# Kernel optimization log

Measured on AMD Instinct MI355X. Metric: run time of the kernel, lower is better.

Reference implementation:

```python
import jax, jax.numpy as jnp
import numpy as np
import math

RIEMANN_ZEROS_IM = (14.134725142, 21.022039639, 25.01085758, 30.424876126, 32.935061588,
    37.586178159, 40.918719012, 43.327073281, 48.005150881, 49.773832478, 52.970321478,
    56.446247697, 59.347044003, 60.831778525, 65.112544048, 67.079810529, 69.546401711,
    72.067157674, 75.704690699, 77.144840069, 79.33737502, 82.910380854, 84.735492981,
    87.425274613, 88.809111208, 92.491899271, 94.651344041, 95.870634228, 98.831194218,
    101.317851006, 103.72553804, 105.446623052)

D_MODEL = 1024
N_HEADS = 16
D_HEAD = D_MODEL // N_HEADS  # 64
N_PAIRS = D_HEAD // 2        # 32

# normalized inverse frequencies: gamma_n / gamma_1, inverted
_gamma = np.asarray(RIEMANN_ZEROS_IM[:N_PAIRS], dtype=np.float32)
INV_FREQ = jnp.asarray(1.0 / (_gamma / _gamma[0]))  # [n_pairs]


def _rotate(x, cos, sin):
    # x: [b,h,n,d_head]; cos/sin: [1,h,n,n_pairs]; interleaved pair rotation
    x1 = x[..., 0::2]
    x2 = x[..., 1::2]
    rx1 = x1 * cos - x2 * sin
    rx2 = x1 * sin + x2 * cos
    return jnp.stack([rx1, rx2], axis=-1).reshape(x.shape)


def setup_inputs() -> dict:
    key = jax.random.key(0)
    k1, k2, k3 = jax.random.split(key, 3)
    b, n = 4, 2048
    x = jax.random.normal(k1, (b, n, D_MODEL), dtype=jnp.float32)
    # torch Linear(d, 3d, bias=False): y = x @ W.T; we store W.T directly
    w_qkv = jax.random.normal(k2, (D_MODEL, 3 * D_MODEL), dtype=jnp.float32) / math.sqrt(D_MODEL)
    w_o = jax.random.normal(k3, (D_MODEL, D_MODEL), dtype=jnp.float32) / math.sqrt(D_MODEL)
    log_scale = jnp.zeros((N_HEADS,), dtype=jnp.float32)
    return {"x": x, "w_qkv": w_qkv, "w_o": w_o, "log_scale": log_scale}


def reference(x, w_qkv, w_o, log_scale):
    b, n, d = x.shape
    qkv = (x @ w_qkv).reshape(b, n, 3, N_HEADS, D_HEAD)
    q, k, v = qkv[:, :, 0], qkv[:, :, 1], qkv[:, :, 2]  # [b,n,h,dh]
    q = q.transpose(0, 2, 1, 3)  # [b,h,n,dh]
    k = k.transpose(0, 2, 1, 3)
    v = v.transpose(0, 2, 1, 3)

    scale = jnp.exp(log_scale)  # [h]
    pos = jnp.arange(n, dtype=jnp.float32)
    # theta: [1,h,n,n_pairs]
    theta = pos[None, None, :, None] * INV_FREQ[None, None, None, :] * scale[None, :, None, None]
    cos, sin = jnp.cos(theta), jnp.sin(theta)
    q = _rotate(q, cos, sin)
    k = _rotate(k, cos, sin)

    scores = jnp.einsum('bhqd,bhkd->bhqk', q, k) / math.sqrt(D_HEAD)
    causal = jnp.tril(jnp.ones((n, n), dtype=bool))
    scores = jnp.where(causal[None, None], scores, -jnp.inf)
    attn = jax.nn.softmax(scores, axis=-1)
    out = jnp.einsum('bhqk,bhkd->bhqd', attn, v)
    out = out.transpose(0, 2, 1, 3).reshape(b, n, d)
    return out @ w_o
```

## Files before the change

kernel.cpp:

```cpp
#include <hip/hip_runtime.h>
#include <hip/hip_bf16.h>

#define B_ 4
#define N_ 2048
#define DM 1024
#define NH 16
#define DH 64

typedef __attribute__((ext_vector_type(8))) __bf16 bf16x8;
typedef __attribute__((ext_vector_type(4))) float f32x4;
typedef __attribute__((ext_vector_type(4))) float float4v;
typedef __attribute__((ext_vector_type(4))) unsigned int uint4v;
typedef __attribute__((ext_vector_type(2))) unsigned int uint2v;
typedef __attribute__((ext_vector_type(4))) unsigned short ushort4v;

__device__ __forceinline__ float bf2f(unsigned short h) {
  union { unsigned int u; float f; } v; v.u = ((unsigned int)h) << 16; return v.f;
}
__device__ __forceinline__ unsigned short f2bf(float f) {
  __bf16 h = (__bf16)f;
  return __builtin_bit_cast(unsigned short, h);
}
__device__ __forceinline__ f32x4 mfma16(bf16x8 a, bf16x8 b, f32x4 c) {
  return __builtin_amdgcn_mfma_f32_16x16x32_bf16(a, b, c, 0, 0, 0);
}
__device__ __forceinline__ void gload_lds16(const void* g, void* l) {
  __builtin_amdgcn_global_load_lds(
      (const __attribute__((address_space(1))) unsigned int*)g,
      (__attribute__((address_space(3))) unsigned int*)l, 16, 0, 0);
}

__constant__ float GAMMA_C[32] = {
  14.134725142f, 21.022039639f, 25.01085758f, 30.424876126f,
  32.935061588f, 37.586178159f, 40.918719012f, 43.327073281f,
  48.005150881f, 49.773832478f, 52.970321478f, 56.446247697f,
  59.347044003f, 60.831778525f, 65.112544048f, 67.079810529f,
  69.546401711f, 72.067157674f, 75.704690699f, 77.144840069f,
  79.33737502f,  82.910380854f, 84.735492981f, 87.425274613f,
  88.809111208f, 92.491899271f, 94.651344041f, 95.870634228f,
  98.831194218f, 101.317851006f, 103.72553804f, 105.446623052f
};

__global__ __launch_bounds__(256) void cast_f32_bf16(
    const float* __restrict__ in, unsigned short* __restrict__ out, int n4) {
  int i = blockIdx.x * 256 + threadIdx.x;
  if (i >= n4) return;
  float4v v = *(const float4v*)&in[(size_t)i * 4];
  ushort4v o;
  o[0] = f2bf(v[0]); o[1] = f2bf(v[1]); o[2] = f2bf(v[2]); o[3] = f2bf(v[3]);
  *(ushort4v*)&out[(size_t)i * 4] = o;
}

__global__ __launch_bounds__(256) void tcast(
    const float* __restrict__ in, unsigned short* __restrict__ out, int K, int N) {
  __shared__ float t[32][33];
  int n0 = blockIdx.x * 32, k0 = blockIdx.y * 32;
  int tx = threadIdx.x, ty = threadIdx.y;
#pragma unroll
  for (int j = 0; j < 4; ++j)
    t[ty + j * 8][tx] = in[(size_t)(k0 + ty + j * 8) * N + n0 + tx];
  __syncthreads();
#pragma unroll
  for (int j = 0; j < 4; ++j)
    out[(size_t)(n0 + ty + j * 8) * K + k0 + tx] = f2bf(t[tx][ty + j * 8]);
}

template <int OUTF32>
__global__ __launch_bounds__(256) void gemm_bt(
    const unsigned short* __restrict__ A, const unsigned short* __restrict__ BT,
    void* __restrict__ C, int M, int N, int K) {
  __shared__ unsigned short As[128 * 32];
  __shared__ unsigned short Bs[128 * 32];
  int tid = threadIdx.x;
  int lane = tid & 63, wid = tid >> 6;
  int wr = wid >> 1, wc = wid & 1;
  int lr = lane & 15, lg = lane >> 4;
  int bm = blockIdx.y * 128, bn = blockIdx.x * 128;
  int srow = lane >> 2, sch = lane & 3;
  f32x4 acc[4][4];
#pragma unroll
  for (int m = 0; m < 4; ++m)
#pragma unroll
    for (int n = 0; n < 4; ++n) acc[m][n] = (f32x4){0.f, 0.f, 0.f, 0.f};

  for (int k0 = 0; k0 < K; k0 += 32) {
    __syncthreads();
#pragma unroll
    for (int it = 0; it < 2; ++it) {
      int rbase = wid * 16 + it * 64;
      gload_lds16(&A[(size_t)(bm + rbase + srow) * K + k0 + sch * 8],
                  &As[rbase * 32]);
      gload_lds16(&BT[(size_t)(bn + rbase + srow) * K + k0 + sch * 8],
                  &Bs[rbase * 32]);
    }
    __syncthreads();
    bf16x8 af[4], bfr[4];
#pragma unroll
    for (int m = 0; m < 4; ++m)
      af[m] = *(const bf16x8*)&As[(wr * 64 + m * 16 + lr) * 32 + lg * 8];
#pragma unroll
    for (int n = 0; n < 4; ++n)
      bfr[n] = *(const bf16x8*)&Bs[(wc * 64 + n * 16 + lr) * 32 + lg * 8];
    __builtin_amdgcn_s_setprio(1);
#pragma unroll
    for (int m = 0; m < 4; ++m)
#pragma unroll
      for (int n = 0; n < 4; ++n)
        acc[m][n] = mfma16(af[m], bfr[n], acc[m][n]);
    __builtin_amdgcn_s_setprio(0);
  }
#pragma unroll
  for (int m = 0; m < 4; ++m)
#pragma unroll
    for (int n = 0; n < 4; ++n) {
      int row = bm + wr * 64 + m * 16 + lg * 4;
      int col = bn + wc * 64 + n * 16 + lr;
#pragma unroll
      for (int r = 0; r < 4; ++r) {
        if (OUTF32)
          ((float*)C)[(size_t)(row + r) * N + col] = acc[m][n][r];
        else
          ((unsigned short*)C)[(size_t)(row + r) * N + col] = f2bf(acc[m][n][r]);
      }
    }
}

__global__ __launch_bounds__(256) void rope_split(
    const unsigned short* __restrict__ qkv, const float* __restrict__ log_scale,
    unsigned short* __restrict__ Qr, unsigned short* __restrict__ Kr,
    unsigned short* __restrict__ Vr) {
  int t = blockIdx.x * 256 + threadIdx.x;
  int p = t & 31, h = (t >> 5) & 15, n = (t >> 9) & 2047, b = t >> 20;
  float ratio = GAMMA_C[p] / GAMMA_C[0];
  float invf = 1.0f / ratio;
  float scale = expf(log_scale[h]);
  float theta = ((float)n * invf) * scale;
  float sn, cs;
  sincosf(theta, &sn, &cs);
  size_t base = (size_t)(b * N_ + n) * (3 * DM) + h * DH + 2 * p;
  unsigned int qu = *(const unsigned int*)&qkv[base];
  unsigned int ku = *(const unsigned int*)&qkv[base + DM];
  unsigned int vu = *(const unsigned int*)&qkv[base + 2 * DM];
  float q1 = bf2f(qu & 0xffffu), q2 = bf2f(qu >> 16);
  float k1 = bf2f(ku & 0xffffu), k2 = bf2f(ku >> 16);
  unsigned int rq = (unsigned int)f2bf(q1 * cs - q2 * sn) |
                    ((unsigned int)f2bf(q1 * sn + q2 * cs) << 16);
  unsigned int rk = (unsigned int)f2bf(k1 * cs - k2 * sn) |
                    ((unsigned int)f2bf(k1 * sn + k2 * cs) << 16);
  size_t ob = (size_t)((b * NH + h) * N_ + n) * DH + 2 * p;
  *(unsigned int*)&Qr[ob] = rq;
  *(unsigned int*)&Kr[ob] = rk;
  *(unsigned int*)&Vr[ob] = vu;
}

__global__ __launch_bounds__(256) void attn_fwd(
    const unsigned short* __restrict__ Q, const unsigned short* __restrict__ K,
    const unsigned short* __restrict__ V, unsigned short* __restrict__ AO) {
  int orig = blockIdx.x;
  int wg = (orig & 7) * 128 + (orig >> 3);
  int i = wg & 15;
  int qt = ((wg >> 5) & 1) ? (15 - i) : i;
  int bh = wg >> 4;
  int b = bh >> 4, h = bh & 15;
  int q0 = qt * 128;
  int tid = threadIdx.x;
  int lane = tid & 63, w = tid >> 6;
  int lr = lane & 15, lg = lane >> 4;

  const unsigned short* Qh = Q + (size_t)bh * N_ * DH;
  const unsigned short* Kh = K + (size_t)bh * N_ * DH;
  const unsigned short* Vh = V + (size_t)bh * N_ * DH;

  __shared__ unsigned short Ks[64 * 64];
  __shared__ unsigned short Vt[64 * 64];
  __shared__ unsigned int PsU[4][32][32];

  bf16x8 qf[2][2];
#pragma unroll
  for (int m = 0; m < 2; ++m)
#pragma unroll
    for (int dh = 0; dh < 2; ++dh)
      qf[m][dh] = *(const bf16x8*)
          &Qh[(size_t)(q0 + w * 32 + m * 16 + lr) * DH + dh * 32 + lg * 8];

  f32x4 oacc[2][4];
#pragma unroll
  for (int m = 0; m < 2; ++m)
#pragma unroll
    for (int nb = 0; nb < 4; ++nb) oacc[m][nb] = (f32x4){0.f, 0.f, 0.f, 0.f};
  float mst[2] = {-1e30f, -1e30f};
  float lst[2] = {0.f, 0.f};

  int wkend = q0 + w * 32 + 31;
  int ksup = q0 + 128;
  int vch = tid & 7, vk = tid >> 3;
  int swz = 4 * (lr & 7);

  for (int k0 = 0; k0 < ksup; k0 += 64) {
    __syncthreads();
#pragma unroll
    for (int it = 0; it < 2; ++it) {
      int rbase = w * 8 + it * 32;
      int row = rbase + (lane >> 3);
      int sk = ((row & 7) ^ (row >> 3)) & 7;
      int ch = lane & 7;
      gload_lds16(&Kh[(size_t)(k0 + row) * DH + ((ch ^ sk) * 8)],
                  &Ks[rbase * 64]);
    }
#pragma unroll
    for (int it = 0; it < 2; ++it) {
      int k = vk + it * 32;
      uint4v vv = *(const uint4v*)&Vh[(size_t)(k0 + k) * DH + vch * 8];
      const unsigned short* pv = (const unsigned short*)&vv;
#pragma unroll
      for (int j = 0; j < 8; ++j) {
        int d = vch * 8 + j;
        int sv = (j ^ vch) & 7;
        Vt[d * 64 + (k ^ (sv << 3))] = pv[j];
      }
    }
    __syncthreads();
    if (k0 > wkend) continue;

    f32x4 s[2][4];
    __builtin_amdgcn_s_setprio(1);
#pragma unroll
    for (int nb = 0; nb < 4; ++nb) {
      int key = nb * 16 + lr;
      int sk = ((key & 7) ^ (key >> 3)) & 7;
      bf16x8 kf0 = *(const bf16x8*)&Ks[key * 64 + ((lg ^ sk) * 8)];
      bf16x8 kf1 = *(const bf16x8*)&Ks[key * 64 + (((4 + lg) ^ sk) * 8)];
#pragma unroll
      for (int m = 0; m < 2; ++m) {
        f32x4 z = (f32x4){0.f, 0.f, 0.f, 0.f};
        z = mfma16(kf0, qf[m][0], z);
        z = mfma16(kf1, qf[m][1], z);
        s[m][nb] = z;
      }
    }
    __builtin_amdgcn_s_setprio(0);

    float sv[2][4][4];
    float mx[2];
#pragma unroll
    for (int m = 0; m < 2; ++m) {
      int qm = q0 + w * 32 + m * 16;
      int q = qm + lr;
      bool um = (k0 + 63 > qm);
#pragma unroll
      for (int nb = 0; nb < 4; ++nb)
#pragma unroll
        for (int r = 0; r < 4; ++r) {
          float t = s[m][nb][r] * 0.125f;
          if (um && (k0 + nb * 16 + lg * 4 + r > q)) t = -1e30f;
          sv[m][nb][r] = t;
        }
      float mx0 = fmaxf(fmaxf(sv[m][0][0], sv[m][0][1]),
                        fmaxf(sv[m][0][2], sv[m][0][3]));
      float mx1 = fmaxf(fmaxf(sv[m][1][0], sv[m][1][1]),
                        fmaxf(sv[m][1][2], sv[m][1][3]));
      float mx2 = fmaxf(fmaxf(sv[m][2][0], sv[m][2][1]),
                        fmaxf(sv[m][2][2], sv[m][2][3]));
      float mx3 = fmaxf(fmaxf(sv[m][3][0], sv[m][3][1]),
                        fmaxf(sv[m][3][2], sv[m][3][3]));
      float m01 = fmaxf(fmaxf(mx0, mx1), fmaxf(mx2, mx3));
      m01 = fmaxf(m01, __shfl_xor(m01, 16, 64));
      m01 = fmaxf(m01, __shfl_xor(m01, 32, 64));
      mx[m] = m01;
    }

    if (__any((mx[0] > mst[0] + 8.f) || (mx[1] > mst[1] + 8.f))) {
      float scs[2];
#pragma unroll
      for (int m = 0; m < 2; ++m) {
        float mnew = fmaxf(mst[m], mx[m]);
        float sc = __expf(mst[m] - mnew);
        mst[m] = mnew;
        lst[m] *= sc;
        scs[m] = sc;
      }
#pragma unroll
      for (int m = 0; m < 2; ++m)
#pragma unroll
        for (int r = 0; r < 4; ++r) {
          float scr = __shfl(scs[m], lg * 4 + r, 64);
#pragma unroll
          for (int nb = 0; nb < 4; ++nb) oacc[m][nb][r] *= scr;
        }
    }

#pragma unroll
    for (int m = 0; m < 2; ++m) {
      float ps = 0.f;
      unsigned int pw[8];
#pragma unroll
      for (int nb = 0; nb < 4; ++nb)
#pragma unroll
        for (int rp = 0; rp < 2; ++rp) {
          float p0 = __expf(sv[m][nb][2 * rp] - mst[m]);
          float p1 = __expf(sv[m][nb][2 * rp + 1] - mst[m]);
          ps += p0 + p1;
          pw[nb * 2 + rp] =
              (unsigned int)f2bf(p0) | ((unsigned int)f2bf(p1) << 16);
        }
#pragma unroll
      for (int nb = 0; nb < 4; ++nb) {
        int c0 = (nb * 8 + lg * 2) ^ swz;
        *(uint2v*)&PsU[w][m * 16 + lr][c0] = (uint2v){pw[nb * 2], pw[nb * 2 + 1]};
      }
      ps += __shfl_xor(ps, 16, 64);
      ps += __shfl_xor(ps, 32, 64);
      lst[m] += ps;
    }
    asm volatile("s_waitcnt lgkmcnt(0)" ::: "memory");
    __builtin_amdgcn_sched_barrier(0);

    __builtin_amdgcn_s_setprio(1);
#pragma unroll
    for (int kh = 0; kh < 2; ++kh) {
      bf16x8 pf0 = *(const bf16x8*)&PsU[w][lr][(kh * 16 + lg * 4) ^ swz];
      bf16x8 pf1 = *(const bf16x8*)&PsU[w][16 + lr][(kh * 16 + lg * 4) ^ swz];
#pragma unroll
      for (int nb = 0; nb < 4; ++nb) {
        int d = nb * 16 + lr;
        int sv2 = ((d & 7) ^ (d >> 3)) & 7;
        bf16x8 vf = *(const bf16x8*)
            &Vt[d * 64 + ((kh * 32 + lg * 8) ^ (sv2 << 3))];
        oacc[0][nb] = mfma16(pf0, vf, oacc[0][nb]);
        oacc[1][nb] = mfma16(pf1, vf, oacc[1][nb]);
      }
    }
    __builtin_amdgcn_s_setprio(0);
  }

#pragma unroll
  for (int m = 0; m < 2; ++m) {
    float inv = 1.0f / lst[m];
#pragma unroll
    for (int r = 0; r < 4; ++r) {
      float invr = __shfl(inv, lg * 4 + r, 64);
      int q = q0 + w * 32 + m * 16 + lg * 4 + r;
#pragma unroll
      for (int nb = 0; nb < 4; ++nb) {
        float o = oacc[m][nb][r] * invr;
        AO[(size_t)(b * N_ + q) * DM + h * DH + nb * 16 + lr] = f2bf(o);
      }
    }
  }
}

extern "C" void kernel_launch(void* const* d_in, const int* in_sizes, int n_in,
                              void* d_out, int out_size, void* d_ws, size_t ws_size,
                              hipStream_t stream) {
  const float* x = (const float*)d_in[0];
  const float* w_qkv = (const float*)d_in[1];
  const float* w_o = (const float*)d_in[2];
  const float* log_scale = (const float*)d_in[3];
  float* out = (float*)d_out;

  char* ws = (char*)d_ws;
  unsigned short* xb  = (unsigned short*)(ws);
  unsigned short* ao  = xb;
  unsigned short* wqT = (unsigned short*)(ws + (16u << 20));
  unsigned short* woT = (unsigned short*)(ws + (22u << 20));
  unsigned short* qkv = (unsigned short*)(ws + (24u << 20));
  unsigned short* Qr  = (unsigned short*)(ws + (72u << 20));
  unsigned short* Kr  = (unsigned short*)(ws + (88u << 20));
  unsigned short* Vr  = (unsigned short*)(ws + (104u << 20));

  cast_f32_bf16<<<8192, 256, 0, stream>>>(x, xb, (B_ * N_ * DM) / 4);
  dim3 tb(32, 8);
  tcast<<<dim3(3 * DM / 32, DM / 32), tb, 0, stream>>>(w_qkv, wqT, DM, 3 * DM);
  tcast<<<dim3(DM / 32, DM / 32), tb, 0, stream>>>(w_o, woT, DM, DM);
  gemm_bt<0><<<dim3(3 * DM / 128, (B_ * N_) / 128), 256, 0, stream>>>(
      xb, wqT, qkv, B_ * N_, 3 * DM, DM);
  rope_split<<<(B_ * N_ * NH * 32) / 256, 256, 0, stream>>>(
      qkv, log_scale, Qr, Kr, Vr);
  attn_fwd<<<B_ * NH * (N_ / 128), 256, 0, stream>>>(Qr, Kr, Vr, ao);
  gemm_bt<1><<<dim3(DM / 128, (B_ * N_) / 128), 256, 0, stream>>>(
      ao, woT, out, B_ * N_, DM, DM);
}
```

Measured before the change: 257.0 us.

## Pre-transpose V in rope kernel and double-buffer K/V tiles in attention

The rope/split kernel now writes V already transposed ([bh][d][n]) through a shared-memory transpose, so attention can load V tiles with async global-to-LDS copies instead of scalar LDS scatter stores. The attention kernel double-buffers the K and V tiles, prefetching the next tile while computing the current one, and drops from two barriers to one per iteration. The P staging buffer is halved by processing the two m-subtiles one after another. The cost is extra LDS for the double buffers, a shared-memory transpose in the rope kernel, and a serialized P write/read per m-subtile.

Result: slower. 265.6 us (+3.4%).

```diff
diff --git a/kernel.cpp b/kernel.cpp
--- a/kernel.cpp
+++ b/kernel.cpp
@@ -128,29 +128,50 @@
 __global__ __launch_bounds__(256) void rope_split(
     const unsigned short* __restrict__ qkv, const float* __restrict__ log_scale,
     unsigned short* __restrict__ Qr, unsigned short* __restrict__ Kr,
-    unsigned short* __restrict__ Vr) {
-  int t = blockIdx.x * 256 + threadIdx.x;
-  int p = t & 31, h = (t >> 5) & 15, n = (t >> 9) & 2047, b = t >> 20;
-  float ratio = GAMMA_C[p] / GAMMA_C[0];
-  float invf = 1.0f / ratio;
-  float scale = expf(log_scale[h]);
-  float theta = ((float)n * invf) * scale;
-  float sn, cs;
-  sincosf(theta, &sn, &cs);
-  size_t base = (size_t)(b * N_ + n) * (3 * DM) + h * DH + 2 * p;
-  unsigned int qu = *(const unsigned int*)&qkv[base];
-  unsigned int ku = *(const unsigned int*)&qkv[base + DM];
-  unsigned int vu = *(const unsigned int*)&qkv[base + 2 * DM];
-  float q1 = bf2f(qu & 0xffffu), q2 = bf2f(qu >> 16);
-  float k1 = bf2f(ku & 0xffffu), k2 = bf2f(ku >> 16);
-  unsigned int rq = (unsigned int)f2bf(q1 * cs - q2 * sn) |
-                    ((unsigned int)f2bf(q1 * sn + q2 * cs) << 16);
-  unsigned int rk = (unsigned int)f2bf(k1 * cs - k2 * sn) |
-                    ((unsigned int)f2bf(k1 * sn + k2 * cs) << 16);
-  size_t ob = (size_t)((b * NH + h) * N_ + n) * DH + 2 * p;
-  *(unsigned int*)&Qr[ob] = rq;
-  *(unsigned int*)&Kr[ob] = rk;
-  *(unsigned int*)&Vr[ob] = vu;
+    unsigned short* __restrict__ Vt) {
+  int nt = blockIdx.x, bh = blockIdx.y;
+  int b = bh >> 4, h = bh & 15;
+  int n0 = nt * 128;
+  int tid = threadIdx.x;
+  int p = tid & 31, nl0 = tid >> 5;
+  __shared__ unsigned int Vl[128][33];
+  float invf = GAMMA_C[0] / GAMMA_C[p];
+  float scale = __expf(log_scale[h]);
+#pragma unroll
+  for (int j = 0; j < 16; ++j) {
+    int nl = nl0 + j * 8;
+    int n = n0 + nl;
+    size_t base = (size_t)(b * N_ + n) * (3 * DM) + h * DH + 2 * p;
+    unsigned int qu = *(const unsigned int*)&qkv[base];
+    unsigned int ku = *(const unsigned int*)&qkv[base + DM];
+    unsigned int vu = *(const unsigned int*)&qkv[base + 2 * DM];
+    float th = (float)n * invf * scale;
+    float sn, cs;
+    sincosf(th, &sn, &cs);
+    float q1 = bf2f(qu & 0xffffu), q2 = bf2f(qu >> 16);
+    float k1 = bf2f(ku & 0xffffu), k2 = bf2f(ku >> 16);
+    unsigned int rq = (unsigned int)f2bf(q1 * cs - q2 * sn) |
+                      ((unsigned int)f2bf(q1 * sn + q2 * cs) << 16);
+    unsigned int rk = (unsigned int)f2bf(k1 * cs - k2 * sn) |
+                      ((unsigned int)f2bf(k1 * sn + k2 * cs) << 16);
+    size_t ob = (size_t)(bh * N_ + n) * DH + 2 * p;
+    *(unsigned int*)&Qr[ob] = rq;
+    *(unsigned int*)&Kr[ob] = rk;
+    Vl[nl][p] = vu;
+  }
+  __syncthreads();
+  int d = tid & 63, ch = tid >> 6;
+  int dp = d >> 1, sh = (d & 1) * 16;
+#pragma unroll
+  for (int j = 0; j < 4; ++j) {
+    int cc = ch + j * 4;
+    unsigned short o[8];
+#pragma unroll
+    for (int i = 0; i < 8; ++i)
+      o[i] = (unsigned short)(Vl[cc * 8 + i][dp] >> sh);
+    *(uint4v*)&Vt[(size_t)bh * DH * N_ + (size_t)d * N_ + n0 + cc * 8] =
+        *(const uint4v*)o;
+  }
 }
 
 __global__ __launch_bounds__(256) void attn_fwd(
@@ -169,11 +190,11 @@
 
   const unsigned short* Qh = Q + (size_t)bh * N_ * DH;
   const unsigned short* Kh = K + (size_t)bh * N_ * DH;
-  const unsigned short* Vh = V + (size_t)bh * N_ * DH;
-
-  __shared__ unsigned short Ks[64 * 64];
-  __shared__ unsigned short Vt[64 * 64];
-  __shared__ unsigned int PsU[4][32][32];
+  const unsigned short* Vh = V + (size_t)bh * DH * N_;
+
+  __shared__ unsigned short Ks[2][64 * 64];
+  __shared__ unsigned short Vs[2][64 * 64];
+  __shared__ unsigned int PsU[4][16][32];
 
   bf16x8 qf[2][2];
 #pragma unroll
@@ -193,144 +214,148 @@
 
   int wkend = q0 + w * 32 + 31;
   int ksup = q0 + 128;
-  int vch = tid & 7, vk = tid >> 3;
   int swz = 4 * (lr & 7);
 
+  int srow = lane >> 3, sch = lane & 7;
+
+#pragma unroll
+  for (int it = 0; it < 2; ++it) {
+    int rbase = w * 16 + it * 8;
+    int row = rbase + srow;
+    int sk = (row & 7) ^ ((row >> 3) & 7);
+    gload_lds16(&Kh[(size_t)row * DH + ((sch ^ sk) * 8)], &Ks[0][rbase * 64]);
+    gload_lds16(&Vh[(size_t)row * N_ + ((sch ^ sk) * 8)], &Vs[0][rbase * 64]);
+  }
+  asm volatile("s_waitcnt vmcnt(0)" ::: "memory");
+  __syncthreads();
+  int cur = 0;
+
   for (int k0 = 0; k0 < ksup; k0 += 64) {
+    if (k0 + 64 < ksup) {
+#pragma unroll
+      for (int it = 0; it < 2; ++it) {
+        int rbase = w * 16 + it * 8;
+        int row = rbase + srow;
+        int sk = (row & 7) ^ ((row >> 3) & 7);
+        gload_lds16(&Kh[(size_t)(k0 + 64 + row) * DH + ((sch ^ sk) * 8)],
+                    &Ks[cur ^ 1][rbase * 64]);
+        gload_lds16(&Vh[(size_t)row * N_ + k0 + 64 + ((sch ^ sk) * 8)],
+                    &Vs[cur ^ 1][rbase * 64]);
+      }
+    }
+
+    if (k0 <= wkend) {
+      f32x4 s[2][4];
+      __builtin_amdgcn_s_setprio(1);
+#pragma unroll
+      for (int nb = 0; nb < 4; ++nb) {
+        int key = nb * 16 + lr;
+        int sk = (key & 7) ^ ((key >> 3) & 7);
+        bf16x8 kf0 = *(const bf16x8*)&Ks[cur][key * 64 + ((lg ^ sk) * 8)];
+        bf16x8 kf1 = *(const bf16x8*)&Ks[cur][key * 64 + (((4 + lg) ^ sk) * 8)];
+#pragma unroll
+        for (int m = 0; m < 2; ++m) {
+          f32x4 z = (f32x4){0.f, 0.f, 0.f, 0.f};
+          z = mfma16(kf0, qf[m][0], z);
+          z = mfma16(kf1, qf[m][1], z);
+          s[m][nb] = z;
+        }
+      }
+      __builtin_amdgcn_s_setprio(0);
+
+      float sv[2][4][4];
+      float mx[2];
+#pragma unroll
+      for (int m = 0; m < 2; ++m) {
+        int qm = q0 + w * 32 + m * 16;
+        int q = qm + lr;
+        bool um = (k0 + 63 > qm);
+#pragma unroll
+        for (int nb = 0; nb < 4; ++nb)
+#pragma unroll
+          for (int r = 0; r < 4; ++r) {
+            float t = s[m][nb][r] * 0.125f;
+            if (um && (k0 + nb * 16 + lg * 4 + r > q)) t = -1e30f;
+            sv[m][nb][r] = t;
+          }
+        float mx0 = fmaxf(fmaxf(sv[m][0][0], sv[m][0][1]),
+                          fmaxf(sv[m][0][2], sv[m][0][3]));
+        float mx1 = fmaxf(fmaxf(sv[m][1][0], sv[m][1][1]),
+                          fmaxf(sv[m][1][2], sv[m][1][3]));
+        float mx2 = fmaxf(fmaxf(sv[m][2][0], sv[m][2][1]),
+                          fmaxf(sv[m][2][2], sv[m][2][3]));
+        float mx3 = fmaxf(fmaxf(sv[m][3][0], sv[m][3][1]),
+                          fmaxf(sv[m][3][2], sv[m][3][3]));
+        float m01 = fmaxf(fmaxf(mx0, mx1), fmaxf(mx2, mx3));
+        m01 = fmaxf(m01, __shfl_xor(m01, 16, 64));
+        m01 = fmaxf(m01, __shfl_xor(m01, 32, 64));
+        mx[m] = m01;
+      }
+
+      if (__any((mx[0] > mst[0] + 8.f) || (mx[1] > mst[1] + 8.f))) {
+        float scs[2];
+#pragma unroll
+        for (int m = 0; m < 2; ++m) {
+          float mnew = fmaxf(mst[m], mx[m]);
+          float sc = __expf(mst[m] - mnew);
+          mst[m] = mnew;
+          lst[m] *= sc;
+          scs[m] = sc;
+        }
+#pragma unroll
+        for (int m = 0; m < 2; ++m)
+#pragma unroll
+          for (int r = 0; r < 4; ++r) {
+            float scr = __shfl(scs[m], lg * 4 + r, 64);
+#pragma unroll
+            for (int nb = 0; nb < 4; ++nb) oacc[m][nb][r] *= scr;
+          }
+      }
+
+#pragma unroll
+      for (int m = 0; m < 2; ++m) {
+        float ps = 0.f;
+        unsigned int pw[8];
+#pragma unroll
+        for (int nb = 0; nb < 4; ++nb)
+#pragma unroll
+          for (int rp = 0; rp < 2; ++rp) {
+            float p0 = __expf(sv[m][nb][2 * rp] - mst[m]);
+            float p1 = __expf(sv[m][nb][2 * rp + 1] - mst[m]);
+            ps += p0 + p1;
+            pw[nb * 2 + rp] =
+                (unsigned int)f2bf(p0) | ((unsigned int)f2bf(p1) << 16);
+          }
+#pragma unroll
+        for (int nb = 0; nb < 4; ++nb) {
+          int c0 = (nb * 8 + lg * 2) ^ swz;
+          *(uint2v*)&PsU[w][lr][c0] = (uint2v){pw[nb * 2], pw[nb * 2 + 1]};
+        }
+        ps += __shfl_xor(ps, 16, 64);
+        ps += __shfl_xor(ps, 32, 64);
+        lst[m] += ps;
+        asm volatile("s_waitcnt lgkmcnt(0)" ::: "memory");
+        __builtin_amdgcn_sched_barrier(0);
+        __builtin_amdgcn_s_setprio(1);
+#pragma unroll
+        for (int kh = 0; kh < 2; ++kh) {
+          bf16x8 pf = *(const bf16x8*)&PsU[w][lr][(kh * 16 + lg * 4) ^ swz];
+#pragma unroll
+          for (int nb = 0; nb < 4; ++nb) {
+            int d = nb * 16 + lr;
+            int sv2 = (d & 7) ^ ((d >> 3) & 7);
+            int c = kh * 4 + lg;
+            bf16x8 vf = *(const bf16x8*)&Vs[cur][d * 64 + ((c ^ sv2) * 8)];
+            oacc[m][nb] = mfma16(pf, vf, oacc[m][nb]);
+          }
+        }
+        __builtin_amdgcn_s_setprio(0);
+      }
+    }
+
+    asm volatile("s_waitcnt vmcnt(0)" ::: "memory");
     __syncthreads();
-#pragma unroll
-    for (int it = 0; it < 2; ++it) {
-      int rbase = w * 8 + it * 32;
-      int row = rbase + (lane >> 3);
-      int sk = ((row & 7) ^ (row >> 3)) & 7;
-      int ch = lane & 7;
-      gload_lds16(&Kh[(size_t)(k0 + row) * DH + ((ch ^ sk) * 8)],
-                  &Ks[rbase * 64]);
-    }
-#pragma unroll
-    for (int it = 0; it < 2; ++it) {
-      int k = vk + it * 32;
-      uint4v vv = *(const uint4v*)&Vh[(size_t)(k0 + k) * DH + vch * 8];
-      const unsigned short* pv = (const unsigned short*)&vv;
-#pragma unroll
-      for (int j = 0; j < 8; ++j) {
-        int d = vch * 8 + j;
-        int sv = (j ^ vch) & 7;
-        Vt[d * 64 + (k ^ (sv << 3))] = pv[j];
-      }
-    }
-    __syncthreads();
-    if (k0 > wkend) continue;
-
-    f32x4 s[2][4];
-    __builtin_amdgcn_s_setprio(1);
-#pragma unroll
-    for (int nb = 0; nb < 4; ++nb) {
-      int key = nb * 16 + lr;
-      int sk = ((key & 7) ^ (key >> 3)) & 7;
-      bf16x8 kf0 = *(const bf16x8*)&Ks[key * 64 + ((lg ^ sk) * 8)];
-      bf16x8 kf1 = *(const bf16x8*)&Ks[key * 64 + (((4 + lg) ^ sk) * 8)];
-#pragma unroll
-      for (int m = 0; m < 2; ++m) {
-        f32x4 z = (f32x4){0.f, 0.f, 0.f, 0.f};
-        z = mfma16(kf0, qf[m][0], z);
-        z = mfma16(kf1, qf[m][1], z);
-        s[m][nb] = z;
-      }
-    }
-    __builtin_amdgcn_s_setprio(0);
-
-    float sv[2][4][4];
-    float mx[2];
-#pragma unroll
-    for (int m = 0; m < 2; ++m) {
-      int qm = q0 + w * 32 + m * 16;
-      int q = qm + lr;
-      bool um = (k0 + 63 > qm);
-#pragma unroll
-      for (int nb = 0; nb < 4; ++nb)
-#pragma unroll
-        for (int r = 0; r < 4; ++r) {
-          float t = s[m][nb][r] * 0.125f;
-          if (um && (k0 + nb * 16 + lg * 4 + r > q)) t = -1e30f;
-          sv[m][nb][r] = t;
-        }
-      float mx0 = fmaxf(fmaxf(sv[m][0][0], sv[m][0][1]),
-                        fmaxf(sv[m][0][2], sv[m][0][3]));
-      float mx1 = fmaxf(fmaxf(sv[m][1][0], sv[m][1][1]),
-                        fmaxf(sv[m][1][2], sv[m][1][3]));
-      float mx2 = fmaxf(fmaxf(sv[m][2][0], sv[m][2][1]),
-                        fmaxf(sv[m][2][2], sv[m][2][3]));
-      float mx3 = fmaxf(fmaxf(sv[m][3][0], sv[m][3][1]),
-                        fmaxf(sv[m][3][2], sv[m][3][3]));
-      float m01 = fmaxf(fmaxf(mx0, mx1), fmaxf(mx2, mx3));
-      m01 = fmaxf(m01, __shfl_xor(m01, 16, 64));
-      m01 = fmaxf(m01, __shfl_xor(m01, 32, 64));
-      mx[m] = m01;
-    }
-
-    if (__any((mx[0] > mst[0] + 8.f) || (mx[1] > mst[1] + 8.f))) {
-      float scs[2];
-#pragma unroll
-      for (int m = 0; m < 2; ++m) {
-        float mnew = fmaxf(mst[m], mx[m]);
-        float sc = __expf(mst[m] - mnew);
-        mst[m] = mnew;
-        lst[m] *= sc;
-        scs[m] = sc;
-      }
-#pragma unroll
-      for (int m = 0; m < 2; ++m)
-#pragma unroll
-        for (int r = 0; r < 4; ++r) {
-          float scr = __shfl(scs[m], lg * 4 + r, 64);
-#pragma unroll
-          for (int nb = 0; nb < 4; ++nb) oacc[m][nb][r] *= scr;
-        }
-    }
-
-#pragma unroll
-    for (int m = 0; m < 2; ++m) {
-      float ps = 0.f;
-      unsigned int pw[8];
-#pragma unroll
-      for (int nb = 0; nb < 4; ++nb)
-#pragma unroll
-        for (int rp = 0; rp < 2; ++rp) {
-          float p0 = __expf(sv[m][nb][2 * rp] - mst[m]);
-          float p1 = __expf(sv[m][nb][2 * rp + 1] - mst[m]);
-          ps += p0 + p1;
-          pw[nb * 2 + rp] =
-              (unsigned int)f2bf(p0) | ((unsigned int)f2bf(p1) << 16);
-        }
-#pragma unroll
-      for (int nb = 0; nb < 4; ++nb) {
-        int c0 = (nb * 8 + lg * 2) ^ swz;
-        *(uint2v*)&PsU[w][m * 16 + lr][c0] = (uint2v){pw[nb * 2], pw[nb * 2 + 1]};
-      }
-      ps += __shfl_xor(ps, 16, 64);
-      ps += __shfl_xor(ps, 32, 64);
-      lst[m] += ps;
-    }
-    asm volatile("s_waitcnt lgkmcnt(0)" ::: "memory");
-    __builtin_amdgcn_sched_barrier(0);
-
-    __builtin_amdgcn_s_setprio(1);
-#pragma unroll
-    for (int kh = 0; kh < 2; ++kh) {
-      bf16x8 pf0 = *(const bf16x8*)&PsU[w][lr][(kh * 16 + lg * 4) ^ swz];
-      bf16x8 pf1 = *(const bf16x8*)&PsU[w][16 + lr][(kh * 16 + lg * 4) ^ swz];
-#pragma unroll
-      for (int nb = 0; nb < 4; ++nb) {
-        int d = nb * 16 + lr;
-        int sv2 = ((d & 7) ^ (d >> 3)) & 7;
-        bf16x8 vf = *(const bf16x8*)
-            &Vt[d * 64 + ((kh * 32 + lg * 8) ^ (sv2 << 3))];
-        oacc[0][nb] = mfma16(pf0, vf, oacc[0][nb]);
-        oacc[1][nb] = mfma16(pf1, vf, oacc[1][nb]);
-      }
-    }
-    __builtin_amdgcn_s_setprio(0);
+    cur ^= 1;
   }
 
 #pragma unroll
@@ -366,7 +391,7 @@
   unsigned short* qkv = (unsigned short*)(ws + (24u << 20));
   unsigned short* Qr  = (unsigned short*)(ws + (72u << 20));
   unsigned short* Kr  = (unsigned short*)(ws + (88u << 20));
-  unsigned short* Vr  = (unsigned short*)(ws + (104u << 20));
+  unsigned short* Vt  = (unsigned short*)(ws + (104u << 20));
 
   cast_f32_bf16<<<8192, 256, 0, stream>>>(x, xb, (B_ * N_ * DM) / 4);
   dim3 tb(32, 8);
@@ -374,9 +399,9 @@
   tcast<<<dim3(DM / 32, DM / 32), tb, 0, stream>>>(w_o, woT, DM, DM);
   gemm_bt<0><<<dim3(3 * DM / 128, (B_ * N_) / 128), 256, 0, stream>>>(
       xb, wqT, qkv, B_ * N_, 3 * DM, DM);
-  rope_split<<<(B_ * N_ * NH * 32) / 256, 256, 0, stream>>>(
-      qkv, log_scale, Qr, Kr, Vr);
-  attn_fwd<<<B_ * NH * (N_ / 128), 256, 0, stream>>>(Qr, Kr, Vr, ao);
+  rope_split<<<dim3(16, B_ * NH), 256, 0, stream>>>(
+      qkv, log_scale, Qr, Kr, Vt);
+  attn_fwd<<<B_ * NH * (N_ / 128), 256, 0, stream>>>(Qr, Kr, Vt, ao);
   gemm_bt<1><<<dim3(DM / 128, (B_ * N_) / 128), 256, 0, stream>>>(
       ao, woT, out, B_ * N_, DM, DM);
 }
```
